# Kernel tuning notes

Measured on AMD Instinct MI355X. Metric: run time of the kernel, lower is better.

## Reference

```python
import jax, jax.numpy as jnp
import numpy as np

MODEL_DIM = 2048
NUM_EXPERTS = 64
CAPACITY_FACTOR = 1.0
NUM_TOKENS = 16384


def setup_inputs() -> dict:
    key = jax.random.key(0)
    k1, k2 = jax.random.split(key)
    inp = jax.random.normal(k1, (NUM_TOKENS, MODEL_DIM), dtype=jnp.float32)
    # wg: Linear(model_dim, num_experts, bias=False) -> weight [num_experts, model_dim]
    wg = jax.random.normal(k2, (NUM_EXPERTS, MODEL_DIM), dtype=jnp.float32) * 0.02
    return {"input": inp, "wg": wg}


def reference(input, wg):
    # logits: [N, E]
    logits = jnp.einsum('nd,ed->ne', input, wg)
    N, E = logits.shape
    # training-mode capacity: capacity_factor * ceil(N / E)
    capacity = int(CAPACITY_FACTOR * ((N + E - 1) // E))

    indices1_s = jnp.argmax(logits, axis=1)                      # [N]
    gates = jax.nn.softmax(logits, axis=1)                       # [N, E]
    mask1 = jax.nn.one_hot(indices1_s, E, dtype=gates.dtype)     # [N, E]
    gates1_s = jnp.sum(gates * mask1, axis=1)                    # [N]

    # fwd_cumsum: exclusive per-expert rank of each token (token order)
    cum = jnp.cumsum(mask1.astype(jnp.int32), axis=0)            # [N, E]
    locations1_s = (cum[jnp.arange(N), indices1_s] - 1).astype(jnp.int32)

    # float32 aux-loss branch
    me = jnp.sum(gates, axis=0)                                  # [E]
    ce = jnp.sum(mask1, axis=0)                                  # [E]
    l_aux = jnp.sum(me * ce) * (E / (N * N))

    return (l_aux, indices1_s.astype(jnp.int32), capacity, locations1_s, gates1_s, E)
```

## Files before the change

kernel.cpp:

```cpp
#include <hip/hip_runtime.h>
#include <hip/hip_bf16.h>

#define N_TOK 16384
#define DIM   2048
#define NEXP  64
#define BM    32
#define BK    64
#define NTILE (DIM / BK)
#define NBLK  (N_TOK / BM)

#define OFF_LAUX  0
#define OFF_IDX   1
#define OFF_CAP   (1 + N_TOK)
#define OFF_LOC   (2 + N_TOK)
#define OFF_GATES (2 + 2 * N_TOK)
#define OFF_E     (2 + 3 * N_TOK)

typedef __attribute__((address_space(1))) const float gfloat;
typedef __attribute__((address_space(3))) float lfloat;

__global__ __launch_bounds__(128)
void gate_gemm_kernel(const float* __restrict__ inp,
                      const float* __restrict__ wg,
                      float* __restrict__ out,
                      float* __restrict__ me,
                      int* __restrict__ hist,
                      int* __restrict__ idx_g,
                      int* __restrict__ rank_g)
{
    __shared__ float a_s[2][BM * BK];
    __shared__ float b_s[2][NEXP * BK];
    __shared__ float lg[BM][NEXP + 1];
    __shared__ float mx_s[BM], rs_s[BM];

    const int tid  = threadIdx.x;
    const int wave = tid >> 6;
    const int lane = tid & 63;
    const int blk  = blockIdx.x;
    const int row0 = blk * BM;
    const int ty   = tid >> 4;
    const int tx   = tid & 15;

    const int lr = lane >> 4;
    const int lk = 4 * (lane & 15);

    float acc[4][4];
    #pragma unroll
    for (int i = 0; i < 4; ++i)
        #pragma unroll
        for (int j = 0; j < 4; ++j) acc[i][j] = 0.f;

    auto stage = [&](int bb, int k0) {
        if (wave == 0) {
            #pragma unroll
            for (int ja = 0; ja < 8; ++ja) {
                const float* src = inp + (size_t)(row0 + 4 * ja + lr) * DIM
                                   + k0 + (lk ^ (ja << 2));
                __builtin_amdgcn_global_load_lds((const gfloat*)src,
                    (lfloat*)&a_s[bb][256 * ja], 16, 0, 0);
            }
            #pragma unroll
            for (int jb = 0; jb < 4; ++jb) {
                const float* src = wg + (size_t)(4 * jb + lr) * DIM
                                   + k0 + (lk ^ ((jb & 7) << 2));
                __builtin_amdgcn_global_load_lds((const gfloat*)src,
                    (lfloat*)&b_s[bb][256 * jb], 16, 0, 0);
            }
        } else {
            #pragma unroll
            for (int jb = 4; jb < 16; ++jb) {
                const float* src = wg + (size_t)(4 * jb + lr) * DIM
                                   + k0 + (lk ^ ((jb & 7) << 2));
                __builtin_amdgcn_global_load_lds((const gfloat*)src,
                    (lfloat*)&b_s[bb][256 * jb], 16, 0, 0);
            }
        }
    };

    stage(0, 0);

    int buf = 0;
    for (int t = 0; t < NTILE; ++t) {
        __syncthreads();
        if (t < NTILE - 1) stage(buf ^ 1, (t + 1) * BK);
        const float* ap = &a_s[buf][0];
        const float* bp = &b_s[buf][0];
        #pragma unroll
        for (int kq = 0; kq < 16; ++kq) {
            float4 av[4], bv[4];
            #pragma unroll
            for (int ii = 0; ii < 4; ++ii) {
                int tt = 4 * ty + ii;
                av[ii] = *reinterpret_cast<const float4*>(
                    &ap[tt * BK + ((4 * kq) ^ ((ty & 7) << 2))]);
            }
            #pragma unroll
            for (int jj = 0; jj < 4; ++jj) {
                int e = 4 * tx + jj;
                bv[jj] = *reinterpret_cast<const float4*>(
                    &bp[e * BK + ((4 * kq) ^ ((tx & 7) << 2))]);
            }
            #pragma unroll
            for (int ii = 0; ii < 4; ++ii)
                #pragma unroll
                for (int jj = 0; jj < 4; ++jj) {
                    acc[ii][jj] += av[ii].x * bv[jj].x;
                    acc[ii][jj] += av[ii].y * bv[jj].y;
                    acc[ii][jj] += av[ii].z * bv[jj].z;
                    acc[ii][jj] += av[ii].w * bv[jj].w;
                }
        }
        buf ^= 1;
    }
    __syncthreads();

    #pragma unroll
    for (int ii = 0; ii < 4; ++ii)
        #pragma unroll
        for (int jj = 0; jj < 4; ++jj)
            lg[4 * ty + ii][4 * tx + jj] = acc[ii][jj];
    __syncthreads();

    int am = 0;
    if (tid < BM) {
        float m = -1e30f;
        for (int e = 0; e < NEXP; ++e) {
            float v = lg[tid][e];
            if (v > m) { m = v; am = e; }
        }
        float s = 0.f;
        for (int e = 0; e < NEXP; ++e)
            s += expf(lg[tid][e] - m);
        float inv = 1.0f / s;
        mx_s[tid] = m;
        rs_s[tid] = inv;
        idx_g[row0 + tid] = am;
        out[OFF_IDX + row0 + tid]   = (float)am;
        out[OFF_GATES + row0 + tid] = inv;
    }
    __syncthreads();

    if (tid < NEXP) {
        float a = 0.f;
        for (int t = 0; t < BM; ++t)
            a += expf(lg[t][tid] - mx_s[t]) * rs_s[t];
        atomicAdd(&me[tid], a);
    }

    if (tid < BM) {
        unsigned long long below = (1ull << tid) - 1ull;
        int rank = 0;
        for (int e = 0; e < NEXP; ++e) {
            unsigned long long bal = __ballot(am == e);
            if (am == e) rank = (int)__popcll(bal & below);
            if (tid == 0) hist[blk * NEXP + e] = (int)__popcll(bal);
        }
        rank_g[row0 + tid] = rank;
    }
}

__global__ __launch_bounds__(1024)
void scan_kernel(const int* __restrict__ hist,
                 int* __restrict__ offs,
                 const float* __restrict__ me,
                 float* __restrict__ out)
{
    __shared__ int part[16][NEXP];
    const int tid = threadIdx.x;
    const int e = tid & 63;
    const int g = tid >> 6;

    int ps = 0;
    for (int i = 0; i < 32; ++i)
        ps += hist[(g * 32 + i) * NEXP + e];
    part[g][e] = ps;
    __syncthreads();

    if (tid < NEXP) {
        int run = 0;
        for (int gg = 0; gg < 16; ++gg) {
            int v = part[gg][e];
            part[gg][e] = run;
            run += v;
        }
        float la = me[e] * (float)run;
        #pragma unroll
        for (int o = 32; o > 0; o >>= 1)
            la += __shfl_down(la, o);
        if (tid == 0) {
            out[OFF_LAUX] = la * 2.384185791015625e-07f;
            out[OFF_CAP]  = 256.0f;
            out[OFF_E]    = 64.0f;
        }
    }
    __syncthreads();

    int run2 = part[g][e];
    for (int i = 0; i < 32; ++i) {
        int b = g * 32 + i;
        offs[b * NEXP + e] = run2;
        run2 += hist[b * NEXP + e];
    }
}

__global__ __launch_bounds__(256)
void loc_kernel(const int* __restrict__ idx_g,
                const int* __restrict__ rank_g,
                const int* __restrict__ offs,
                float* __restrict__ out)
{
    int t = blockIdx.x * 256 + threadIdx.x;
    int e = idx_g[t];
    int b = t >> 5;
    out[OFF_LOC + t] = (float)(rank_g[t] + offs[b * NEXP + e]);
}

extern "C" void kernel_launch(void* const* d_in, const int* in_sizes, int n_in,
                              void* d_out, int out_size, void* d_ws, size_t ws_size,
                              hipStream_t stream)
{
    const float* inp = (const float*)d_in[0];
    const float* wg  = (const float*)d_in[1];
    float* out = (float*)d_out;

    float* me   = (float*)d_ws;
    int* hist   = (int*)d_ws + NEXP;
    int* offs   = hist + NBLK * NEXP;
    int* idx_g  = offs + NBLK * NEXP;
    int* rank_g = idx_g + N_TOK;

    hipMemsetAsync(me, 0, NEXP * sizeof(float), stream);

    hipLaunchKernelGGL(gate_gemm_kernel, dim3(NBLK), dim3(128), 0, stream,
                       inp, wg, out, me, hist, idx_g, rank_g);
    hipLaunchKernelGGL(scan_kernel, dim3(1), dim3(1024), 0, stream,
                       hist, offs, me, out);
    hipLaunchKernelGGL(loc_kernel, dim3(N_TOK / 256), dim3(256), 0, stream,
                       idx_g, rank_g, offs, out);
}
```

Baseline: 271.7 us.

## Split-K gate GEMM across four waves with per-wave LDS staging and block-level reductions

Restructures the gate GEMM so each of four waves handles a quarter of the K dimension. Each wave stages only its own input rows into LDS with per-wave vmcnt waits instead of block barriers, and reads gate weights directly from global/L2 rather than staging them. Partial logits are reduced through LDS, and the softmax, argmax and expert-probability sums are computed with wave shuffles across 8 lanes per token. The global atomic on `me` and its memset are replaced by per-block partials that the scan kernel reduces. The trade-off is more global traffic for the weights and an extra split-K reduction, in exchange for fewer barriers and more threads per block.

```diff
diff --git a/kernel.cpp b/kernel.cpp
--- a/kernel.cpp
+++ b/kernel.cpp
@@ -5,8 +5,10 @@
 #define DIM   2048
 #define NEXP  64
 #define BM    32
-#define BK    64
-#define NTILE (DIM / BK)
+#define KS    4
+#define KW    (DIM / KS)
+#define CK    64
+#define NCH   (KW / CK)
 #define NBLK  (N_TOK / BM)
 
 #define OFF_LAUX  0
@@ -19,135 +21,150 @@
 typedef __attribute__((address_space(1))) const float gfloat;
 typedef __attribute__((address_space(3))) float lfloat;
 
-__global__ __launch_bounds__(128)
+__global__ __launch_bounds__(256)
 void gate_gemm_kernel(const float* __restrict__ inp,
                       const float* __restrict__ wg,
                       float* __restrict__ out,
-                      float* __restrict__ me,
+                      float* __restrict__ me_p,
                       int* __restrict__ hist,
                       int* __restrict__ idx_g,
                       int* __restrict__ rank_g)
 {
-    __shared__ float a_s[2][BM * BK];
-    __shared__ float b_s[2][NEXP * BK];
-    __shared__ float lg[BM][NEXP + 1];
-    __shared__ float mx_s[BM], rs_s[BM];
+    __shared__ float a_s[KS][2][BM * CK];
+    __shared__ float me_s[NEXP];
+    __shared__ int   am_s[BM];
 
     const int tid  = threadIdx.x;
-    const int wave = tid >> 6;
+    const int w    = tid >> 6;
     const int lane = tid & 63;
+    const int tg   = lane >> 4;
+    const int eg   = lane & 15;
     const int blk  = blockIdx.x;
     const int row0 = blk * BM;
-    const int ty   = tid >> 4;
-    const int tx   = tid & 15;
-
-    const int lr = lane >> 4;
-    const int lk = 4 * (lane & 15);
-
-    float acc[4][4];
-    #pragma unroll
-    for (int i = 0; i < 4; ++i)
-        #pragma unroll
-        for (int j = 0; j < 4; ++j) acc[i][j] = 0.f;
-
-    auto stage = [&](int bb, int k0) {
-        if (wave == 0) {
+
+    const float4* wg4 = reinterpret_cast<const float4*>(wg);
+
+    float acc[8][4];
+    #pragma unroll
+    for (int m = 0; m < 8; ++m)
+        #pragma unroll
+        for (int j = 0; j < 4; ++j) acc[m][j] = 0.f;
+
+    auto stage = [&](int bb, int c) {
+        const int kbase = w * KW + c * CK;
+        #pragma unroll
+        for (int j = 0; j < 8; ++j) {
+            const int tj  = 4 * j + (lane >> 4);
+            const int tgj = tj >> 3;
+            const float* src = inp + (size_t)(row0 + tj) * DIM
+                               + kbase + 4 * ((lane & 15) ^ tgj);
+            __builtin_amdgcn_global_load_lds((const gfloat*)src,
+                (lfloat*)&a_s[w][bb][j * 256], 16, 0, 0);
+        }
+    };
+
+    stage(0, 0);
+
+    int buf = 0;
+    for (int c = 0; c < NCH; ++c) {
+        if (c < NCH - 1) {
+            stage(buf ^ 1, c + 1);
+            asm volatile("s_waitcnt vmcnt(8)" ::: "memory");
+        } else {
+            asm volatile("s_waitcnt vmcnt(0)" ::: "memory");
+        }
+        const float* ab = &a_s[w][buf][0];
+        const int kg0 = (w * KW + c * CK) >> 2;
+        #pragma unroll 4
+        for (int kq = 0; kq < 16; ++kq) {
+            float4 bv[4];
             #pragma unroll
-            for (int ja = 0; ja < 8; ++ja) {
-                const float* src = inp + (size_t)(row0 + 4 * ja + lr) * DIM
-                                   + k0 + (lk ^ (ja << 2));
-                __builtin_amdgcn_global_load_lds((const gfloat*)src,
-                    (lfloat*)&a_s[bb][256 * ja], 16, 0, 0);
+            for (int j = 0; j < 4; ++j)
+                bv[j] = wg4[(4 * eg + j) * (DIM / 4) + kg0 + kq];
+            const int ak = 4 * (kq ^ tg);
+            #pragma unroll
+            for (int m = 0; m < 8; ++m) {
+                float4 av = *reinterpret_cast<const float4*>(
+                    &ab[(8 * tg + m) * CK + ak]);
+                #pragma unroll
+                for (int j = 0; j < 4; ++j)
+                    acc[m][j] += av.x * bv[j].x + av.y * bv[j].y
+                               + av.z * bv[j].z + av.w * bv[j].w;
             }
-            #pragma unroll
-            for (int jb = 0; jb < 4; ++jb) {
-                const float* src = wg + (size_t)(4 * jb + lr) * DIM
-                                   + k0 + (lk ^ ((jb & 7) << 2));
-                __builtin_amdgcn_global_load_lds((const gfloat*)src,
-                    (lfloat*)&b_s[bb][256 * jb], 16, 0, 0);
-            }
-        } else {
-            #pragma unroll
-            for (int jb = 4; jb < 16; ++jb) {
-                const float* src = wg + (size_t)(4 * jb + lr) * DIM
-                                   + k0 + (lk ^ ((jb & 7) << 2));
-                __builtin_amdgcn_global_load_lds((const gfloat*)src,
-                    (lfloat*)&b_s[bb][256 * jb], 16, 0, 0);
-            }
-        }
-    };
-
-    stage(0, 0);
-
-    int buf = 0;
-    for (int t = 0; t < NTILE; ++t) {
-        __syncthreads();
-        if (t < NTILE - 1) stage(buf ^ 1, (t + 1) * BK);
-        const float* ap = &a_s[buf][0];
-        const float* bp = &b_s[buf][0];
-        #pragma unroll
-        for (int kq = 0; kq < 16; ++kq) {
-            float4 av[4], bv[4];
-            #pragma unroll
-            for (int ii = 0; ii < 4; ++ii) {
-                int tt = 4 * ty + ii;
-                av[ii] = *reinterpret_cast<const float4*>(
-                    &ap[tt * BK + ((4 * kq) ^ ((ty & 7) << 2))]);
-            }
-            #pragma unroll
-            for (int jj = 0; jj < 4; ++jj) {
-                int e = 4 * tx + jj;
-                bv[jj] = *reinterpret_cast<const float4*>(
-                    &bp[e * BK + ((4 * kq) ^ ((tx & 7) << 2))]);
-            }
-            #pragma unroll
-            for (int ii = 0; ii < 4; ++ii)
-                #pragma unroll
-                for (int jj = 0; jj < 4; ++jj) {
-                    acc[ii][jj] += av[ii].x * bv[jj].x;
-                    acc[ii][jj] += av[ii].y * bv[jj].y;
-                    acc[ii][jj] += av[ii].z * bv[jj].z;
-                    acc[ii][jj] += av[ii].w * bv[jj].w;
-                }
         }
         buf ^= 1;
     }
-    __syncthreads();
-
-    #pragma unroll
-    for (int ii = 0; ii < 4; ++ii)
-        #pragma unroll
-        for (int jj = 0; jj < 4; ++jj)
-            lg[4 * ty + ii][4 * tx + jj] = acc[ii][jj];
-    __syncthreads();
-
-    int am = 0;
+
+    __syncthreads();
+    if (tid < NEXP) me_s[tid] = 0.f;
+
+    float* part = &a_s[0][0][0];
+    #pragma unroll
+    for (int m = 0; m < 8; ++m) {
+        const int t = 8 * tg + m;
+        float4 v = make_float4(acc[m][0], acc[m][1], acc[m][2], acc[m][3]);
+        *reinterpret_cast<float4*>(&part[(w * BM + t) * NEXP + 4 * eg]) = v;
+    }
+    __syncthreads();
+
+    const int tok = tid >> 3;
+    const int e0  = (tid & 7) * 8;
+    float lgv[8];
+    #pragma unroll
+    for (int h = 0; h < 8; ++h) lgv[h] = 0.f;
+    #pragma unroll
+    for (int w2 = 0; w2 < KS; ++w2) {
+        #pragma unroll
+        for (int q = 0; q < 2; ++q) {
+            float4 p = *reinterpret_cast<const float4*>(
+                &part[(w2 * BM + tok) * NEXP + e0 + 4 * q]);
+            lgv[4 * q + 0] += p.x; lgv[4 * q + 1] += p.y;
+            lgv[4 * q + 2] += p.z; lgv[4 * q + 3] += p.w;
+        }
+    }
+
+    float mx = lgv[0]; int ai = e0;
+    #pragma unroll
+    for (int h = 1; h < 8; ++h)
+        if (lgv[h] > mx) { mx = lgv[h]; ai = e0 + h; }
+    #pragma unroll
+    for (int d = 1; d < 8; d <<= 1) {
+        float om = __shfl_xor(mx, d);
+        int   oi = __shfl_xor(ai, d);
+        if (om > mx || (om == mx && oi < ai)) { mx = om; ai = oi; }
+    }
+    float pv[8], s = 0.f;
+    #pragma unroll
+    for (int h = 0; h < 8; ++h) { pv[h] = expf(lgv[h] - mx); s += pv[h]; }
+    #pragma unroll
+    for (int d = 1; d < 8; d <<= 1) s += __shfl_xor(s, d);
+    const float inv = 1.0f / s;
+
+    float mep[8];
+    #pragma unroll
+    for (int h = 0; h < 8; ++h) mep[h] = pv[h] * inv;
+    #pragma unroll
+    for (int d = 8; d < 64; d <<= 1)
+        #pragma unroll
+        for (int h = 0; h < 8; ++h) mep[h] += __shfl_xor(mep[h], d);
+    if (lane < 8) {
+        #pragma unroll
+        for (int h = 0; h < 8; ++h)
+            atomicAdd(&me_s[lane * 8 + h], mep[h]);
+    }
+
+    if ((tid & 7) == 0) {
+        am_s[tok] = ai;
+        idx_g[row0 + tok] = ai;
+        out[OFF_IDX + row0 + tok]   = (float)ai;
+        out[OFF_GATES + row0 + tok] = inv;
+    }
+    __syncthreads();
+
+    if (tid < NEXP) me_p[blk * NEXP + tid] = me_s[tid];
+
     if (tid < BM) {
-        float m = -1e30f;
-        for (int e = 0; e < NEXP; ++e) {
-            float v = lg[tid][e];
-            if (v > m) { m = v; am = e; }
-        }
-        float s = 0.f;
-        for (int e = 0; e < NEXP; ++e)
-            s += expf(lg[tid][e] - m);
-        float inv = 1.0f / s;
-        mx_s[tid] = m;
-        rs_s[tid] = inv;
-        idx_g[row0 + tid] = am;
-        out[OFF_IDX + row0 + tid]   = (float)am;
-        out[OFF_GATES + row0 + tid] = inv;
-    }
-    __syncthreads();
-
-    if (tid < NEXP) {
-        float a = 0.f;
-        for (int t = 0; t < BM; ++t)
-            a += expf(lg[t][tid] - mx_s[t]) * rs_s[t];
-        atomicAdd(&me[tid], a);
-    }
-
-    if (tid < BM) {
+        const int am = am_s[tid];
         unsigned long long below = (1ull << tid) - 1ull;
         int rank = 0;
         for (int e = 0; e < NEXP; ++e) {
@@ -162,28 +179,34 @@
 __global__ __launch_bounds__(1024)
 void scan_kernel(const int* __restrict__ hist,
                  int* __restrict__ offs,
-                 const float* __restrict__ me,
+                 const float* __restrict__ me_p,
                  float* __restrict__ out)
 {
-    __shared__ int part[16][NEXP];
+    __shared__ int   part[16][NEXP];
+    __shared__ float pme[16][NEXP];
     const int tid = threadIdx.x;
     const int e = tid & 63;
     const int g = tid >> 6;
 
-    int ps = 0;
-    for (int i = 0; i < 32; ++i)
-        ps += hist[(g * 32 + i) * NEXP + e];
+    int ps = 0; float ms = 0.f;
+    for (int i = 0; i < 32; ++i) {
+        const int b = g * 32 + i;
+        ps += hist[b * NEXP + e];
+        ms += me_p[b * NEXP + e];
+    }
     part[g][e] = ps;
+    pme[g][e]  = ms;
     __syncthreads();
 
     if (tid < NEXP) {
-        int run = 0;
+        int run = 0; float me = 0.f;
         for (int gg = 0; gg < 16; ++gg) {
-            int v = part[gg][e];
+            const int v = part[gg][e];
             part[gg][e] = run;
             run += v;
-        }
-        float la = me[e] * (float)run;
+            me  += pme[gg][e];
+        }
+        float la = me * (float)run;
         #pragma unroll
         for (int o = 32; o > 0; o >>= 1)
             la += __shfl_down(la, o);
@@ -197,7 +220,7 @@
 
     int run2 = part[g][e];
     for (int i = 0; i < 32; ++i) {
-        int b = g * 32 + i;
+        const int b = g * 32 + i;
         offs[b * NEXP + e] = run2;
         run2 += hist[b * NEXP + e];
     }
@@ -223,18 +246,16 @@
     const float* wg  = (const float*)d_in[1];
     float* out = (float*)d_out;
 
-    float* me   = (float*)d_ws;
-    int* hist   = (int*)d_ws + NEXP;
+    float* me_p = (float*)d_ws;
+    int* hist   = (int*)d_ws + NBLK * NEXP;
     int* offs   = hist + NBLK * NEXP;
     int* idx_g  = offs + NBLK * NEXP;
     int* rank_g = idx_g + N_TOK;
 
-    hipMemsetAsync(me, 0, NEXP * sizeof(float), stream);
-
-    hipLaunchKernelGGL(gate_gemm_kernel, dim3(NBLK), dim3(128), 0, stream,
-                       inp, wg, out, me, hist, idx_g, rank_g);
+    hipLaunchKernelGGL(gate_gemm_kernel, dim3(NBLK), dim3(256), 0, stream,
+                       inp, wg, out, me_p, hist, idx_g, rank_g);
     hipLaunchKernelGGL(scan_kernel, dim3(1), dim3(1024), 0, stream,
-                       hist, offs, me, out);
+                       hist, offs, me_p, out);
     hipLaunchKernelGGL(loc_kernel, dim3(N_TOK / 256), dim3(256), 0, stream,
                        idx_g, rank_g, offs, out);
 }
```

New measurement: 302.8 us. +11.5%, slower.
